# Kernel tuning notes

Measured on AMD Instinct MI355X. Metric: run time of the kernel, lower is better.

Reference implementation:

```python
import jax, jax.numpy as jnp
import numpy as np

BS, C, H, W = 2, 256, 64, 64
CH = C // 8  # hidden channels = 32


def conv1(x, w, b):
    # 1x1 conv: w [out,in], b [out], x [b,in,H,W] -> [b,out,H,W]
    return jnp.einsum('oc,bchw->bohw', w, x) + b[None, :, None, None]


def setup_inputs() -> dict:
    key = jax.random.key(0)
    ks = jax.random.split(key, 32)
    d = {}
    d['x'] = jax.random.normal(ks[0], (BS, C, H, W), dtype=jnp.float32)
    d['y'] = jax.random.normal(ks[1], (BS, C, H, W), dtype=jnp.float32)
    i = 2
    def wproj(shape):
        nonlocal i
        w = jax.random.normal(ks[i], shape, dtype=jnp.float32) * 0.05
        i += 1
        return w
    for nm in ['f1', 'g1', 'h1', 'f2', 'g2', 'h2']:
        d['w' + nm] = wproj((CH, C))
        d['b' + nm] = jnp.zeros((CH,), dtype=jnp.float32)
    for nm in ['v11', 'v12', 'v21', 'v22']:
        d['w' + nm] = wproj((C, CH))
        d['b' + nm] = jnp.zeros((C,), dtype=jnp.float32)
    for nm in ['o1', 'o2']:
        d['w' + nm] = wproj((C, 2 * C))
        d['b' + nm] = jnp.zeros((C,), dtype=jnp.float32)
    return d


def reference(x, y, wf1, bf1, wg1, bg1, wh1, bh1, wf2, bf2, wg2, bg2, wh2, bh2,
              wv11, bv11, wv12, bv12, wv21, bv21, wv22, bv22, wo1, bo1, wo2, bo2):
    bs, c, h, w = x.shape
    n = h * w
    f1 = conv1(x, wf1, bf1).reshape(bs, -1, n)  # [b,ch,n]
    g1 = conv1(x, wg1, bg1).reshape(bs, -1, n)
    f2 = conv1(y, wf2, bf2).reshape(bs, -1, n)
    g2 = conv1(y, wg2, bg2).reshape(bs, -1, n)
    # attn = softmax(f^T g) over last dim, [b,n,n]
    attn11 = jax.nn.softmax(jnp.einsum('bcn,bcm->bnm', f1, g1), axis=-1)
    attn12 = jax.nn.softmax(jnp.einsum('bcn,bcm->bnm', f1, g2), axis=-1)
    attn21 = jax.nn.softmax(jnp.einsum('bcn,bcm->bnm', f2, g1), axis=-1)
    attn22 = jax.nn.softmax(jnp.einsum('bcn,bcm->bnm', f2, g2), axis=-1)
    h1 = conv1(x, wh1, bh1).reshape(bs, -1, n)  # note: both h from x, as in source
    h2 = conv1(x, wh2, bh2).reshape(bs, -1, n)
    # bmm(h, attn^T): out[c,m] = sum_n h[c,n] attn[m,n]
    v11 = conv1(jnp.einsum('bcn,bmn->bcm', h1, attn11).reshape(bs, -1, h, w), wv11, bv11)
    v12 = conv1(jnp.einsum('bcn,bmn->bcm', h2, attn12).reshape(bs, -1, h, w), wv12, bv12)
    v21 = conv1(jnp.einsum('bcn,bmn->bcm', h1, attn21).reshape(bs, -1, h, w), wv21, bv21)
    v22 = conv1(jnp.einsum('bcn,bmn->bcm', h2, attn22).reshape(bs, -1, h, w), wv22, bv22)
    x_out = x + conv1(jnp.concatenate([v11, v12], axis=1), wo1, bo1)
    y_out = y + conv1(jnp.concatenate([v21, v22], axis=1), wo2, bo2)
    return (x_out, y_out)
```

## Files before the change

kernel.cpp:

```cpp
#include <hip/hip_runtime.h>
#include <hip/hip_bf16.h>
#include <cstdint>

#define N 4096
#define CC 256
#define CH 32
#define L2E 1.4426950408889634f

typedef __attribute__((ext_vector_type(8)))  short short8;
typedef __attribute__((ext_vector_type(16))) float f32x16;
typedef __attribute__((ext_vector_type(4)))  uint32_t u32x4;

#define OFF_WFRAG 0
#define OFF_WOT   49152
#define OFF_WEFF  311296
#define OFF_BEFF  344064
#define OFF_QF    344576
#define OFF_KF    606720
#define OFF_VF    868864
#define OFF_AOT   1131008

__device__ __forceinline__ uint32_t cvtpk_bf16(float lo, float hi) {
  uint32_t r;
  asm("v_cvt_pk_bf16_f32 %0, %1, %2" : "=v"(r) : "v"(lo), "v"(hi));
  return r;
}

__device__ __forceinline__ void rows_to_frags(const float* p, u32x4& lo, u32x4& hi) {
#pragma unroll
  for (int kh = 0; kh < 2; ++kh) {
    int base = kh * 8;
    uint32_t x0 = cvtpk_bf16(p[base + 0], p[base + 1]);
    uint32_t y0 = cvtpk_bf16(p[base + 4], p[base + 5]);
    asm volatile("v_permlane32_swap_b32 %0, %1" : "+v"(x0), "+v"(y0));
    uint32_t x1 = cvtpk_bf16(p[base + 2], p[base + 3]);
    uint32_t y1 = cvtpk_bf16(p[base + 6], p[base + 7]);
    asm volatile("v_permlane32_swap_b32 %0, %1" : "+v"(x1), "+v"(y1));
    u32x4 r; r[0] = x0; r[1] = x1; r[2] = y0; r[3] = y1;
    if (kh == 0) lo = r; else hi = r;
  }
}

__global__ void k_prep(const float* __restrict__ wf1, const float* __restrict__ wg1,
                       const float* __restrict__ wh1, const float* __restrict__ wf2,
                       const float* __restrict__ wg2, const float* __restrict__ wh2,
                       const float* __restrict__ wo1, const float* __restrict__ wo2,
                       uint16_t* __restrict__ wfragb, float* __restrict__ wot) {
  int bid = blockIdx.x;
  if (bid < 192) {
    int idx = bid * 256 + threadIdx.x;
    int q = idx >> 13, kb = (idx >> 9) & 15, l = (idx >> 3) & 63, j = idx & 7;
    int ch = l & 31, c = kb * 16 + (l >> 5) * 8 + j;
    const float* w = q == 0 ? wf1 : q == 1 ? wg1 : q == 2 ? wh1
                   : q == 3 ? wf2 : q == 4 ? wg2 : wh2;
    wfragb[idx] = (uint16_t)cvtpk_bf16(w[ch * CC + c], 0.f);
  } else {
    int idx = (bid - 192) * 256 + threadIdx.x;
    int o = idx & 255, j = (idx >> 8) & 511, r = idx >> 17;
    const float* wo = r == 0 ? wo1 : wo2;
    wot[idx] = wo[o * 512 + j];
  }
}

__global__ void k_weff(const float* __restrict__ wot,
                       const float* __restrict__ wv11, const float* __restrict__ wv12,
                       const float* __restrict__ wv21, const float* __restrict__ wv22,
                       const float* __restrict__ bv11, const float* __restrict__ bv12,
                       const float* __restrict__ bv21, const float* __restrict__ bv22,
                       const float* __restrict__ bo1, const float* __restrict__ bo2,
                       float* __restrict__ weff, float* __restrict__ beff) {
  int bid = blockIdx.x;
  int o = threadIdx.x;
  if (bid < 128) {
    int r = bid >> 6, ch = bid & 63, half = ch >> 5, chp = ch & 31;
    const float* wv = (r == 0) ? (half ? wv12 : wv11) : (half ? wv22 : wv21);
    const float* wocol = wot + ((size_t)r * 512 + half * 256) * 256 + o;
    float a[8];
#pragma unroll
    for (int u = 0; u < 8; ++u) a[u] = 0.f;
#pragma unroll 4
    for (int c = 0; c < 256; c += 8) {
#pragma unroll
      for (int u = 0; u < 8; ++u)
        a[u] = fmaf(wocol[(size_t)(c + u) * 256], wv[(c + u) * CH + chp], a[u]);
    }
    weff[((size_t)r * 64 + ch) * 256 + o] =
        ((a[0] + a[1]) + (a[2] + a[3])) + ((a[4] + a[5]) + (a[6] + a[7]));
  } else {
    int r = bid - 128;
    const float* bo  = r == 0 ? bo1 : bo2;
    const float* bva = r == 0 ? bv11 : bv21;
    const float* bvb = r == 0 ? bv12 : bv22;
    const float* wocol = wot + (size_t)r * 512 * 256 + o;
    float a[4], b4[4];
#pragma unroll
    for (int u = 0; u < 4; ++u) { a[u] = 0.f; b4[u] = 0.f; }
#pragma unroll 8
    for (int c = 0; c < 256; c += 4) {
#pragma unroll
      for (int u = 0; u < 4; ++u) {
        a[u]  = fmaf(wocol[(size_t)(c + u) * 256],       bva[c + u], a[u]);
        b4[u] = fmaf(wocol[(size_t)(c + u + 256) * 256], bvb[c + u], b4[u]);
      }
    }
    beff[r * 256 + o] = bo[o] + ((a[0] + a[1]) + (a[2] + a[3]))
                              + ((b4[0] + b4[1]) + (b4[2] + b4[3]));
  }
}

__global__ __launch_bounds__(256) void k_proj(
    const float* __restrict__ x, const float* __restrict__ y,
    const uint16_t* __restrict__ wfragb,
    const float* __restrict__ bf1, const float* __restrict__ bg1, const float* __restrict__ bh1,
    const float* __restrict__ bf2, const float* __restrict__ bg2, const float* __restrict__ bh2,
    uint16_t* __restrict__ Qf, uint16_t* __restrict__ Kf, uint16_t* __restrict__ Vf) {
  int bid = blockIdx.x;
  int w = __builtin_amdgcn_readfirstlane(threadIdx.x >> 6);
  int l = threadIdx.x & 63, l31 = l & 31, l5 = l >> 5;

  int q, ql, b, nt, inst;
  const float* src;
  const float* bias;
  bool isf, isV;
  if (bid < 256) {
    ql = w; b = bid >> 7; nt = bid & 127;
    src = x; inst = 0;
    q = (ql == 3) ? 5 : ql;
    isf = (ql == 0); isV = (ql >= 2);
    bias = ql == 0 ? bf1 : ql == 1 ? bg1 : ql == 2 ? bh1 : bh2;
  } else {
    int u = (bid - 256) * 4 + w;
    int chunk = u >> 1; ql = u & 1;
    b = chunk >> 7; nt = chunk & 127;
    src = y; inst = 1;
    q = 3 + ql;
    isf = (ql == 0); isV = false;
    bias = ql == 0 ? bf2 : bg2;
  }

  const u32x4* wp = (const u32x4*)wfragb + (size_t)q * 16 * 64 + l;
  u32x4 wfr[16];
#pragma unroll
  for (int kb = 0; kb < 16; ++kb) wfr[kb] = wp[kb * 64];

  const float* sp = src + (size_t)b * CC * N + (size_t)(l5 * 8) * N + nt * 32 + l31;
  f32x16 acc;
#pragma unroll
  for (int r = 0; r < 16; ++r) acc[r] = 0.f;

  if (isV) {
#pragma unroll
    for (int kb = 0; kb < 16; ++kb) {
      const float* kp = sp + (size_t)kb * 16 * N;
      float xj[8];
#pragma unroll
      for (int j = 0; j < 8; ++j) xj[j] = kp[(size_t)j * N];
      u32x4 bu;
#pragma unroll
      for (int jh = 0; jh < 4; ++jh) bu[jh] = cvtpk_bf16(xj[2 * jh], xj[2 * jh + 1]);
      acc = __builtin_amdgcn_mfma_f32_32x32x16_bf16(
          __builtin_bit_cast(short8, bu), __builtin_bit_cast(short8, wfr[kb]), acc, 0, 0, 0);
    }
  } else {
#pragma unroll
    for (int kb = 0; kb < 16; ++kb) {
      const float* kp = sp + (size_t)kb * 16 * N;
      float xj[8];
#pragma unroll
      for (int j = 0; j < 8; ++j) xj[j] = kp[(size_t)j * N];
      u32x4 bu;
#pragma unroll
      for (int jh = 0; jh < 4; ++jh) bu[jh] = cvtpk_bf16(xj[2 * jh], xj[2 * jh + 1]);
      acc = __builtin_amdgcn_mfma_f32_32x32x16_bf16(
          __builtin_bit_cast(short8, wfr[kb]), __builtin_bit_cast(short8, bu), acc, 0, 0, 0);
    }
  }

  float p[16];
  if (isV) {
    float bv = bias[l31];
#pragma unroll
    for (int r = 0; r < 16; ++r) p[r] = acc[r] + bv;
  } else {
#pragma unroll
    for (int r = 0; r < 16; ++r) {
      int crow = (r & 3) + 8 * (r >> 2) + 4 * l5;
      float t = acc[r] + bias[crow];
      p[r] = isf ? t * L2E : t;
    }
  }

  u32x4 lo, hi;
  rows_to_frags(p, lo, hi);

  uint16_t* dstb = isV ? Vf : (isf ? Qf : Kf);
  int oinst = isV ? (ql - 2) : inst;
  int b128 = (oinst * 2 + b) * 128 + nt;
  uint32_t* d0 = (uint32_t*)dstb + (size_t)b128 * 512 + l * 4;
  *(u32x4*)d0 = lo;
  *(u32x4*)(d0 + 256) = hi;
}

__global__ __launch_bounds__(512) void k_attn3(const uint16_t* __restrict__ Qf,
                                               const uint16_t* __restrict__ Kf,
                                               const uint16_t* __restrict__ Vf,
                                               float* __restrict__ aot) {
  __shared__ float redAO[8][32][33];
  __shared__ float redL[8][32];
  int bid = blockIdx.x;
  int qt = bid & 127, b = (bid >> 7) & 1, i = bid >> 8;
  int ia = i >> 1, ik = i & 1;
  int tid = threadIdx.x, w = tid >> 6, l = tid & 63, l31 = l & 31, l5 = l >> 5;

  const uint16_t* Qp = Qf + (size_t)((ia * 2 + b) * 128 + qt) * 1024 + l * 8;
  const uint16_t* Kp = Kf + (size_t)((ik * 2 + b) * 128 + w * 16) * 1024 + l * 8;
  const uint16_t* Vp = Vf + (size_t)((ik * 2 + b) * 128 + w * 16) * 1024 + l * 8;

  short8 bq0 = *(const short8*)(Qp);
  short8 bq1 = *(const short8*)(Qp + 512);

  f32x16 zero16, ao;
#pragma unroll
  for (int r = 0; r < 16; ++r) { zero16[r] = 0.f; ao[r] = 0.f; }
  float lacc = 0.f;

  for (int t = 0; t < 16; ++t) {
    const uint16_t* kt = Kp + t * 1024;
    short8 ak0 = *(const short8*)(kt);
    short8 ak1 = *(const short8*)(kt + 512);
    const uint16_t* vt = Vp + t * 1024;
    short8 bv0 = *(const short8*)(vt);
    short8 bv1 = *(const short8*)(vt + 512);

    f32x16 sa = __builtin_amdgcn_mfma_f32_32x32x16_bf16(ak0, bq0, zero16, 0, 0, 0);
    sa = __builtin_amdgcn_mfma_f32_32x32x16_bf16(ak1, bq1, sa, 0, 0, 0);

    float p[16];
#pragma unroll
    for (int r = 0; r < 16; ++r) p[r] = __builtin_amdgcn_exp2f(sa[r]);

    float t0 = 0.f, t1 = 0.f;
#pragma unroll
    for (int r = 0; r < 8; ++r) { t0 += p[2 * r]; t1 += p[2 * r + 1]; }
    lacc += t0 + t1;

    uint32_t wreg[8];
#pragma unroll
    for (int kh = 0; kh < 2; ++kh) {
      int base = kh * 8;
      uint32_t x0 = cvtpk_bf16(p[base + 0], p[base + 1]);
      uint32_t y0 = cvtpk_bf16(p[base + 4], p[base + 5]);
      asm volatile("v_permlane32_swap_b32 %0, %1" : "+v"(x0), "+v"(y0));
      uint32_t x1 = cvtpk_bf16(p[base + 2], p[base + 3]);
      uint32_t y1 = cvtpk_bf16(p[base + 6], p[base + 7]);
      asm volatile("v_permlane32_swap_b32 %0, %1" : "+v"(x1), "+v"(y1));
      wreg[kh * 4 + 0] = x0; wreg[kh * 4 + 1] = x1; wreg[kh * 4 + 2] = y0; wreg[kh * 4 + 3] = y1;
    }
    short8 pa0, pa1;
    {
      u32x4 u0 = {wreg[0], wreg[1], wreg[2], wreg[3]};
      u32x4 u1 = {wreg[4], wreg[5], wreg[6], wreg[7]};
      pa0 = __builtin_bit_cast(short8, u0);
      pa1 = __builtin_bit_cast(short8, u1);
    }
    ao = __builtin_amdgcn_mfma_f32_32x32x16_bf16(pa0, bv0, ao, 0, 0, 0);
    ao = __builtin_amdgcn_mfma_f32_32x32x16_bf16(pa1, bv1, ao, 0, 0, 0);
  }

#pragma unroll
  for (int r = 0; r < 16; ++r) {
    int row = (r & 3) + 8 * (r >> 2) + 4 * l5;
    redAO[w][row][l31] = ao[r];
  }
  lacc += __shfl_xor(lacc, 32);
  if (l < 32) redL[w][l31] = lacc;
  __syncthreads();

  int q5 = tid & 31, chb = tid >> 5;
  float lsum = 0.f;
#pragma unroll
  for (int ww = 0; ww < 8; ++ww) lsum += redL[ww][q5];
  float inv = __builtin_amdgcn_rcpf(lsum);
  float s0 = 0.f, s1 = 0.f;
#pragma unroll
  for (int ww = 0; ww < 8; ++ww) {
    s0 += redAO[ww][q5][chb];
    s1 += redAO[ww][q5][chb + 16];
  }
  int ib = i * 2 + b;
  float* ob = aot + (size_t)ib * CH * N + qt * 32 + q5;
  ob[(size_t)chb * N] = s0 * inv;
  ob[(size_t)(chb + 16) * N] = s1 * inv;
}

__global__ __launch_bounds__(64) void k_epi(const float* __restrict__ x, const float* __restrict__ y,
                                            const float* __restrict__ aot,
                                            const float* __restrict__ weff,
                                            const float* __restrict__ beff,
                                            float* __restrict__ out) {
  int bid = blockIdx.x;
  int mt = bid & 63, og = (bid >> 6) & 15, b = (bid >> 10) & 1, r = bid >> 11;
  int m = mt * 64 + threadIdx.x;
  int o0 = og * 16;
  const float* src = r == 0 ? x : y;
  const float* A0 = aot + (size_t)(r * 4 + b) * CH * N;
  const float* A1 = aot + (size_t)(r * 4 + 2 + b) * CH * N;
  const float* wrow = weff + (size_t)r * 64 * 256;
  float acc[16];
#pragma unroll
  for (int j = 0; j < 16; ++j) acc[j] = 0.f;
#pragma unroll 4
  for (int ch = 0; ch < 32; ++ch) {
    float av = A0[(size_t)ch * N + m];
    const float* wr = wrow + ch * 256 + o0;
#pragma unroll
    for (int j = 0; j < 16; ++j) acc[j] = fmaf(wr[j], av, acc[j]);
  }
#pragma unroll 4
  for (int ch = 0; ch < 32; ++ch) {
    float av = A1[(size_t)ch * N + m];
    const float* wr = wrow + (32 + ch) * 256 + o0;
#pragma unroll
    for (int j = 0; j < 16; ++j) acc[j] = fmaf(wr[j], av, acc[j]);
  }
  float* outr = out + (size_t)r * 2 * CC * N;
#pragma unroll
  for (int j = 0; j < 16; ++j) {
    int o = o0 + j;
    size_t off = ((size_t)b * CC + o) * N + m;
    outr[off] = src[off] + acc[j] + beff[r * CC + o];
  }
}

extern "C" void kernel_launch(void* const* d_in, const int* in_sizes, int n_in,
                              void* d_out, int out_size, void* d_ws, size_t ws_size,
                              hipStream_t stream) {
  const float* x    = (const float*)d_in[0];
  const float* y    = (const float*)d_in[1];
  const float* wf1  = (const float*)d_in[2];
  const float* bf1  = (const float*)d_in[3];
  const float* wg1  = (const float*)d_in[4];
  const float* bg1  = (const float*)d_in[5];
  const float* wh1  = (const float*)d_in[6];
  const float* bh1  = (const float*)d_in[7];
  const float* wf2  = (const float*)d_in[8];
  const float* bf2  = (const float*)d_in[9];
  const float* wg2  = (const float*)d_in[10];
  const float* bg2  = (const float*)d_in[11];
  const float* wh2  = (const float*)d_in[12];
  const float* bh2  = (const float*)d_in[13];
  const float* wv11 = (const float*)d_in[14];
  const float* bv11 = (const float*)d_in[15];
  const float* wv12 = (const float*)d_in[16];
  const float* bv12 = (const float*)d_in[17];
  const float* wv21 = (const float*)d_in[18];
  const float* bv21 = (const float*)d_in[19];
  const float* wv22 = (const float*)d_in[20];
  const float* bv22 = (const float*)d_in[21];
  const float* wo1  = (const float*)d_in[22];
  const float* bo1  = (const float*)d_in[23];
  const float* wo2  = (const float*)d_in[24];
  const float* bo2  = (const float*)d_in[25];

  float* ws   = (float*)d_ws;
  uint16_t* wfragb = (uint16_t*)(ws + OFF_WFRAG);
  float* wot  = ws + OFF_WOT;
  float* weff = ws + OFF_WEFF;
  float* beff = ws + OFF_BEFF;
  uint16_t* Qf = (uint16_t*)(ws + OFF_QF);
  uint16_t* Kf = (uint16_t*)(ws + OFF_KF);
  uint16_t* Vf = (uint16_t*)(ws + OFF_VF);
  float* aot  = ws + OFF_AOT;
  float* out  = (float*)d_out;

  k_prep<<<1216, 256, 0, stream>>>(wf1, wg1, wh1, wf2, wg2, wh2, wo1, wo2, wfragb, wot);
  k_weff<<<130, 256, 0, stream>>>(wot, wv11, wv12, wv21, wv22,
                                  bv11, bv12, bv21, bv22, bo1, bo2, weff, beff);
  k_proj<<<384, 256, 0, stream>>>(x, y, wfragb, bf1, bg1, bh1, bf2, bg2, bh2, Qf, Kf, Vf);
  k_attn3<<<1024, 512, 0, stream>>>(Qf, Kf, Vf, aot);
  k_epi<<<4096, 64, 0, stream>>>(x, y, aot, weff, beff, out);
}
```

Before: 77.72 us.

## Fuse attention with output epilogue and merge weight prep kernels

Merges the weight transpose and effective-weight kernels into one prep kernel that reads wo rows directly instead of a transposed copy. Fuses attention with the output projection epilogue. Each block handles two query tiles for both key sources, reduces the partial sums in LDS, normalizes them, and applies the 64x256 effective weight before writing the residual output. This removes the intermediate aot round-trip and two launches. In exchange the attention grid drops from 1024 to 256 blocks, and the LDS footprint grows, which lowers parallelism and occupancy.

```diff
diff --git a/kernel.cpp b/kernel.cpp
--- a/kernel.cpp
+++ b/kernel.cpp
@@ -12,13 +12,11 @@
 typedef __attribute__((ext_vector_type(4)))  uint32_t u32x4;
 
 #define OFF_WFRAG 0
-#define OFF_WOT   49152
 #define OFF_WEFF  311296
 #define OFF_BEFF  344064
 #define OFF_QF    344576
 #define OFF_KF    606720
 #define OFF_VF    868864
-#define OFF_AOT   1131008
 
 __device__ __forceinline__ uint32_t cvtpk_bf16(float lo, float hi) {
   uint32_t r;
@@ -41,11 +39,35 @@
   }
 }
 
-__global__ void k_prep(const float* __restrict__ wf1, const float* __restrict__ wg1,
-                       const float* __restrict__ wh1, const float* __restrict__ wf2,
-                       const float* __restrict__ wg2, const float* __restrict__ wh2,
-                       const float* __restrict__ wo1, const float* __restrict__ wo2,
-                       uint16_t* __restrict__ wfragb, float* __restrict__ wot) {
+__device__ __forceinline__ void attn_step(short8 ak0, short8 ak1, short8 bv0, short8 bv1,
+                                          short8 bq0, short8 bq1,
+                                          f32x16& ao, float& lacc, const f32x16& zero16) {
+  f32x16 sa = __builtin_amdgcn_mfma_f32_32x32x16_bf16(ak0, bq0, zero16, 0, 0, 0);
+  sa = __builtin_amdgcn_mfma_f32_32x32x16_bf16(ak1, bq1, sa, 0, 0, 0);
+  float p[16];
+#pragma unroll
+  for (int r = 0; r < 16; ++r) p[r] = __builtin_amdgcn_exp2f(sa[r]);
+  float t0 = 0.f, t1 = 0.f;
+#pragma unroll
+  for (int r = 0; r < 8; ++r) { t0 += p[2 * r]; t1 += p[2 * r + 1]; }
+  lacc += t0 + t1;
+  u32x4 lo, hi;
+  rows_to_frags(p, lo, hi);
+  ao = __builtin_amdgcn_mfma_f32_32x32x16_bf16(__builtin_bit_cast(short8, lo), bv0, ao, 0, 0, 0);
+  ao = __builtin_amdgcn_mfma_f32_32x32x16_bf16(__builtin_bit_cast(short8, hi), bv1, ao, 0, 0, 0);
+}
+
+__global__ void k_prep2(const float* __restrict__ wf1, const float* __restrict__ wg1,
+                        const float* __restrict__ wh1, const float* __restrict__ wf2,
+                        const float* __restrict__ wg2, const float* __restrict__ wh2,
+                        const float* __restrict__ wo1, const float* __restrict__ wo2,
+                        const float* __restrict__ wv11, const float* __restrict__ wv12,
+                        const float* __restrict__ wv21, const float* __restrict__ wv22,
+                        const float* __restrict__ bv11, const float* __restrict__ bv12,
+                        const float* __restrict__ bv21, const float* __restrict__ bv22,
+                        const float* __restrict__ bo1, const float* __restrict__ bo2,
+                        uint16_t* __restrict__ wfragb, float* __restrict__ weff,
+                        float* __restrict__ beff) {
   int bid = blockIdx.x;
   if (bid < 192) {
     int idx = bid * 256 + threadIdx.x;
@@ -54,27 +76,12 @@
     const float* w = q == 0 ? wf1 : q == 1 ? wg1 : q == 2 ? wh1
                    : q == 3 ? wf2 : q == 4 ? wg2 : wh2;
     wfragb[idx] = (uint16_t)cvtpk_bf16(w[ch * CC + c], 0.f);
-  } else {
-    int idx = (bid - 192) * 256 + threadIdx.x;
-    int o = idx & 255, j = (idx >> 8) & 511, r = idx >> 17;
-    const float* wo = r == 0 ? wo1 : wo2;
-    wot[idx] = wo[o * 512 + j];
-  }
-}
-
-__global__ void k_weff(const float* __restrict__ wot,
-                       const float* __restrict__ wv11, const float* __restrict__ wv12,
-                       const float* __restrict__ wv21, const float* __restrict__ wv22,
-                       const float* __restrict__ bv11, const float* __restrict__ bv12,
-                       const float* __restrict__ bv21, const float* __restrict__ bv22,
-                       const float* __restrict__ bo1, const float* __restrict__ bo2,
-                       float* __restrict__ weff, float* __restrict__ beff) {
-  int bid = blockIdx.x;
-  int o = threadIdx.x;
-  if (bid < 128) {
-    int r = bid >> 6, ch = bid & 63, half = ch >> 5, chp = ch & 31;
+  } else if (bid < 320) {
+    int bid2 = bid - 192;
+    int r = bid2 >> 6, ch = bid2 & 63, half = ch >> 5, chp = ch & 31;
+    int o = threadIdx.x;
     const float* wv = (r == 0) ? (half ? wv12 : wv11) : (half ? wv22 : wv21);
-    const float* wocol = wot + ((size_t)r * 512 + half * 256) * 256 + o;
+    const float* wrow = (r == 0 ? wo1 : wo2) + (size_t)o * 512 + half * 256;
     float a[8];
 #pragma unroll
     for (int u = 0; u < 8; ++u) a[u] = 0.f;
@@ -82,16 +89,17 @@
     for (int c = 0; c < 256; c += 8) {
 #pragma unroll
       for (int u = 0; u < 8; ++u)
-        a[u] = fmaf(wocol[(size_t)(c + u) * 256], wv[(c + u) * CH + chp], a[u]);
+        a[u] = fmaf(wrow[c + u], wv[(c + u) * CH + chp], a[u]);
     }
     weff[((size_t)r * 64 + ch) * 256 + o] =
         ((a[0] + a[1]) + (a[2] + a[3])) + ((a[4] + a[5]) + (a[6] + a[7]));
   } else {
-    int r = bid - 128;
+    int r = bid - 320;
+    int o = threadIdx.x;
     const float* bo  = r == 0 ? bo1 : bo2;
     const float* bva = r == 0 ? bv11 : bv21;
     const float* bvb = r == 0 ? bv12 : bv22;
-    const float* wocol = wot + (size_t)r * 512 * 256 + o;
+    const float* wrow = (r == 0 ? wo1 : wo2) + (size_t)o * 512;
     float a[4], b4[4];
 #pragma unroll
     for (int u = 0; u < 4; ++u) { a[u] = 0.f; b4[u] = 0.f; }
@@ -99,8 +107,8 @@
     for (int c = 0; c < 256; c += 4) {
 #pragma unroll
       for (int u = 0; u < 4; ++u) {
-        a[u]  = fmaf(wocol[(size_t)(c + u) * 256],       bva[c + u], a[u]);
-        b4[u] = fmaf(wocol[(size_t)(c + u + 256) * 256], bvb[c + u], b4[u]);
+        a[u]  = fmaf(wrow[c + u],       bva[c + u], a[u]);
+        b4[u] = fmaf(wrow[c + u + 256], bvb[c + u], b4[u]);
       }
     }
     beff[r * 256 + o] = bo[o] + ((a[0] + a[1]) + (a[2] + a[3]))
@@ -201,134 +209,100 @@
   *(u32x4*)(d0 + 256) = hi;
 }
 
-__global__ __launch_bounds__(512) void k_attn3(const uint16_t* __restrict__ Qf,
-                                               const uint16_t* __restrict__ Kf,
-                                               const uint16_t* __restrict__ Vf,
-                                               float* __restrict__ aot) {
-  __shared__ float redAO[8][32][33];
-  __shared__ float redL[8][32];
+__global__ __launch_bounds__(512) void k_attnepi(const uint16_t* __restrict__ Qf,
+                                                 const uint16_t* __restrict__ Kf,
+                                                 const uint16_t* __restrict__ Vf,
+                                                 const float* __restrict__ x,
+                                                 const float* __restrict__ y,
+                                                 const float* __restrict__ weff,
+                                                 const float* __restrict__ beff,
+                                                 float* __restrict__ out) {
+  __shared__ float redAO[2][2][4][32][33];
+  __shared__ float redL[2][2][4][32];
+  __shared__ float AN[64][65];
   int bid = blockIdx.x;
-  int qt = bid & 127, b = (bid >> 7) & 1, i = bid >> 8;
-  int ia = i >> 1, ik = i & 1;
-  int tid = threadIdx.x, w = tid >> 6, l = tid & 63, l31 = l & 31, l5 = l >> 5;
-
-  const uint16_t* Qp = Qf + (size_t)((ia * 2 + b) * 128 + qt) * 1024 + l * 8;
-  const uint16_t* Kp = Kf + (size_t)((ik * 2 + b) * 128 + w * 16) * 1024 + l * 8;
-  const uint16_t* Vp = Vf + (size_t)((ik * 2 + b) * 128 + w * 16) * 1024 + l * 8;
-
-  short8 bq0 = *(const short8*)(Qp);
-  short8 bq1 = *(const short8*)(Qp + 512);
-
-  f32x16 zero16, ao;
-#pragma unroll
-  for (int r = 0; r < 16; ++r) { zero16[r] = 0.f; ao[r] = 0.f; }
-  float lacc = 0.f;
-
-  for (int t = 0; t < 16; ++t) {
+  int qg = bid & 63, rb = bid >> 6, r = rb >> 1, b = rb & 1;
+  int tid = threadIdx.x;
+  int w = __builtin_amdgcn_readfirstlane(tid >> 6);
+  int ik = w >> 2, kw = w & 3;
+  int l = tid & 63, l31 = l & 31, l5 = l >> 5;
+  int qt0 = qg * 2, qt1 = qg * 2 + 1;
+
+  const uint16_t* Qp0 = Qf + (size_t)((r * 2 + b) * 128 + qt0) * 1024 + l * 8;
+  const uint16_t* Qp1 = Qf + (size_t)((r * 2 + b) * 128 + qt1) * 1024 + l * 8;
+  const uint16_t* Kp = Kf + (size_t)((ik * 2 + b) * 128 + kw * 32) * 1024 + l * 8;
+  const uint16_t* Vp = Vf + (size_t)((ik * 2 + b) * 128 + kw * 32) * 1024 + l * 8;
+
+  short8 bq00 = *(const short8*)(Qp0);
+  short8 bq01 = *(const short8*)(Qp0 + 512);
+  short8 bq10 = *(const short8*)(Qp1);
+  short8 bq11 = *(const short8*)(Qp1 + 512);
+
+  f32x16 zero16, ao0, ao1;
+#pragma unroll
+  for (int rr = 0; rr < 16; ++rr) { zero16[rr] = 0.f; ao0[rr] = 0.f; ao1[rr] = 0.f; }
+  float lacc0 = 0.f, lacc1 = 0.f;
+
+  for (int t = 0; t < 32; ++t) {
     const uint16_t* kt = Kp + t * 1024;
     short8 ak0 = *(const short8*)(kt);
     short8 ak1 = *(const short8*)(kt + 512);
     const uint16_t* vt = Vp + t * 1024;
     short8 bv0 = *(const short8*)(vt);
     short8 bv1 = *(const short8*)(vt + 512);
-
-    f32x16 sa = __builtin_amdgcn_mfma_f32_32x32x16_bf16(ak0, bq0, zero16, 0, 0, 0);
-    sa = __builtin_amdgcn_mfma_f32_32x32x16_bf16(ak1, bq1, sa, 0, 0, 0);
-
-    float p[16];
-#pragma unroll
-    for (int r = 0; r < 16; ++r) p[r] = __builtin_amdgcn_exp2f(sa[r]);
-
-    float t0 = 0.f, t1 = 0.f;
-#pragma unroll
-    for (int r = 0; r < 8; ++r) { t0 += p[2 * r]; t1 += p[2 * r + 1]; }
-    lacc += t0 + t1;
-
-    uint32_t wreg[8];
-#pragma unroll
-    for (int kh = 0; kh < 2; ++kh) {
-      int base = kh * 8;
-      uint32_t x0 = cvtpk_bf16(p[base + 0], p[base + 1]);
-      uint32_t y0 = cvtpk_bf16(p[base + 4], p[base + 5]);
-      asm volatile("v_permlane32_swap_b32 %0, %1" : "+v"(x0), "+v"(y0));
-      uint32_t x1 = cvtpk_bf16(p[base + 2], p[base + 3]);
-      uint32_t y1 = cvtpk_bf16(p[base + 6], p[base + 7]);
-      asm volatile("v_permlane32_swap_b32 %0, %1" : "+v"(x1), "+v"(y1));
-      wreg[kh * 4 + 0] = x0; wreg[kh * 4 + 1] = x1; wreg[kh * 4 + 2] = y0; wreg[kh * 4 + 3] = y1;
-    }
-    short8 pa0, pa1;
-    {
-      u32x4 u0 = {wreg[0], wreg[1], wreg[2], wreg[3]};
-      u32x4 u1 = {wreg[4], wreg[5], wreg[6], wreg[7]};
-      pa0 = __builtin_bit_cast(short8, u0);
-      pa1 = __builtin_bit_cast(short8, u1);
-    }
-    ao = __builtin_amdgcn_mfma_f32_32x32x16_bf16(pa0, bv0, ao, 0, 0, 0);
-    ao = __builtin_amdgcn_mfma_f32_32x32x16_bf16(pa1, bv1, ao, 0, 0, 0);
-  }
-
-#pragma unroll
-  for (int r = 0; r < 16; ++r) {
-    int row = (r & 3) + 8 * (r >> 2) + 4 * l5;
-    redAO[w][row][l31] = ao[r];
-  }
-  lacc += __shfl_xor(lacc, 32);
-  if (l < 32) redL[w][l31] = lacc;
+    attn_step(ak0, ak1, bv0, bv1, bq00, bq01, ao0, lacc0, zero16);
+    attn_step(ak0, ak1, bv0, bv1, bq10, bq11, ao1, lacc1, zero16);
+  }
+
+#pragma unroll
+  for (int rr = 0; rr < 16; ++rr) {
+    int row = (rr & 3) + 8 * (rr >> 2) + 4 * l5;
+    redAO[ik][0][kw][row][l31] = ao0[rr];
+    redAO[ik][1][kw][row][l31] = ao1[rr];
+  }
+  lacc0 += __shfl_xor(lacc0, 32);
+  lacc1 += __shfl_xor(lacc1, 32);
+  if (l < 32) {
+    redL[ik][0][kw][l31] = lacc0;
+    redL[ik][1][kw][l31] = lacc1;
+  }
   __syncthreads();
 
-  int q5 = tid & 31, chb = tid >> 5;
-  float lsum = 0.f;
-#pragma unroll
-  for (int ww = 0; ww < 8; ++ww) lsum += redL[ww][q5];
-  float inv = __builtin_amdgcn_rcpf(lsum);
-  float s0 = 0.f, s1 = 0.f;
-#pragma unroll
-  for (int ww = 0; ww < 8; ++ww) {
-    s0 += redAO[ww][q5][chb];
-    s1 += redAO[ww][q5][chb + 16];
-  }
-  int ib = i * 2 + b;
-  float* ob = aot + (size_t)ib * CH * N + qt * 32 + q5;
-  ob[(size_t)chb * N] = s0 * inv;
-  ob[(size_t)(chb + 16) * N] = s1 * inv;
-}
-
-__global__ __launch_bounds__(64) void k_epi(const float* __restrict__ x, const float* __restrict__ y,
-                                            const float* __restrict__ aot,
-                                            const float* __restrict__ weff,
-                                            const float* __restrict__ beff,
-                                            float* __restrict__ out) {
-  int bid = blockIdx.x;
-  int mt = bid & 63, og = (bid >> 6) & 15, b = (bid >> 10) & 1, r = bid >> 11;
-  int m = mt * 64 + threadIdx.x;
-  int o0 = og * 16;
+  {
+    int ch = tid >> 3, mblk = tid & 7;
+    int qi = mblk >> 2, mq0 = (mblk & 3) * 8;
+    int ikc = ch >> 5, chp = ch & 31;
+#pragma unroll
+    for (int mm = 0; mm < 8; ++mm) {
+      int mq = mq0 + mm;
+      float L = redL[ikc][qi][0][mq] + redL[ikc][qi][1][mq]
+              + redL[ikc][qi][2][mq] + redL[ikc][qi][3][mq];
+      float s = redAO[ikc][qi][0][mq][chp] + redAO[ikc][qi][1][mq][chp]
+              + redAO[ikc][qi][2][mq][chp] + redAO[ikc][qi][3][mq][chp];
+      AN[ch][qi * 32 + mq] = s * __builtin_amdgcn_rcpf(L);
+    }
+  }
+  __syncthreads();
+
+  int m = tid & 63;
+  int m0 = qg * 64;
+  float acc[32];
+#pragma unroll
+  for (int j = 0; j < 32; ++j) acc[j] = 0.f;
+  const float* wrow = weff + (size_t)(r * 64) * 256 + w * 32;
+  for (int ch = 0; ch < 64; ++ch) {
+    float a = AN[ch][m];
+    const float* wr = wrow + (size_t)ch * 256;
+#pragma unroll
+    for (int j = 0; j < 32; ++j) acc[j] = fmaf(wr[j], a, acc[j]);
+  }
   const float* src = r == 0 ? x : y;
-  const float* A0 = aot + (size_t)(r * 4 + b) * CH * N;
-  const float* A1 = aot + (size_t)(r * 4 + 2 + b) * CH * N;
-  const float* wrow = weff + (size_t)r * 64 * 256;
-  float acc[16];
-#pragma unroll
-  for (int j = 0; j < 16; ++j) acc[j] = 0.f;
-#pragma unroll 4
-  for (int ch = 0; ch < 32; ++ch) {
-    float av = A0[(size_t)ch * N + m];
-    const float* wr = wrow + ch * 256 + o0;
-#pragma unroll
-    for (int j = 0; j < 16; ++j) acc[j] = fmaf(wr[j], av, acc[j]);
-  }
-#pragma unroll 4
-  for (int ch = 0; ch < 32; ++ch) {
-    float av = A1[(size_t)ch * N + m];
-    const float* wr = wrow + (32 + ch) * 256 + o0;
-#pragma unroll
-    for (int j = 0; j < 16; ++j) acc[j] = fmaf(wr[j], av, acc[j]);
-  }
   float* outr = out + (size_t)r * 2 * CC * N;
-#pragma unroll
-  for (int j = 0; j < 16; ++j) {
-    int o = o0 + j;
-    size_t off = ((size_t)b * CC + o) * N + m;
-    outr[off] = src[off] + acc[j] + beff[r * CC + o];
+  const float* be = beff + r * 256 + w * 32;
+#pragma unroll
+  for (int j = 0; j < 32; ++j) {
+    size_t off = ((size_t)b * CC + w * 32 + j) * N + m0 + m;
+    outr[off] = src[off] + acc[j] + be[j];
   }
 }
 
@@ -364,19 +338,17 @@
 
   float* ws   = (float*)d_ws;
   uint16_t* wfragb = (uint16_t*)(ws + OFF_WFRAG);
-  float* wot  = ws + OFF_WOT;
   float* weff = ws + OFF_WEFF;
   float* beff = ws + OFF_BEFF;
   uint16_t* Qf = (uint16_t*)(ws + OFF_QF);
   uint16_t* Kf = (uint16_t*)(ws + OFF_KF);
   uint16_t* Vf = (uint16_t*)(ws + OFF_VF);
-  float* aot  = ws + OFF_AOT;
   float* out  = (float*)d_out;
 
-  k_prep<<<1216, 256, 0, stream>>>(wf1, wg1, wh1, wf2, wg2, wh2, wo1, wo2, wfragb, wot);
-  k_weff<<<130, 256, 0, stream>>>(wot, wv11, wv12, wv21, wv22,
-                                  bv11, bv12, bv21, bv22, bo1, bo2, weff, beff);
+  k_prep2<<<322, 256, 0, stream>>>(wf1, wg1, wh1, wf2, wg2, wh2, wo1, wo2,
+                                   wv11, wv12, wv21, wv22,
+                                   bv11, bv12, bv21, bv22, bo1, bo2,
+                                   wfragb, weff, beff);
   k_proj<<<384, 256, 0, stream>>>(x, y, wfragb, bf1, bg1, bh1, bf2, bg2, bh2, Qf, Kf, Vf);
-  k_attn3<<<1024, 512, 0, stream>>>(Qf, Kf, Vf, aot);
-  k_epi<<<4096, 64, 0, stream>>>(x, y, aot, weff, beff, out);
-}
+  k_attnepi<<<256, 512, 0, stream>>>(Qf, Kf, Vf, x, y, weff, beff, out);
+}
```

After: 78.90 us. About the same (+1.5%).
